# Kernel tuning notes

Hardware: AMD Instinct MI355X
Metric: run time of the kernel (lower is better)

The kernel has to match this reference:

```python
import jax, jax.numpy as jnp
import numpy as np

EMB_DIM = 1024
HEAD_DIM = 64


def setup_inputs() -> dict:
    key = jax.random.key(0)
    kx, kq, kk, kv = jax.random.split(key, 4)
    B, S = 4, 4096
    x = jax.random.normal(kx, (B, S, EMB_DIM), dtype=jnp.float32)
    # nn.Linear weights are [out, in]; kaiming-uniform-ish init scale
    lim = 1.0 / np.sqrt(EMB_DIM)
    Wq = jax.random.uniform(kq, (HEAD_DIM, EMB_DIM), jnp.float32, -lim, lim)
    Wk = jax.random.uniform(kk, (HEAD_DIM, EMB_DIM), jnp.float32, -lim, lim)
    Wv = jax.random.uniform(kv, (HEAD_DIM, EMB_DIM), jnp.float32, -lim, lim)
    return {"x": x, "Wq": Wq, "Wk": Wk, "Wv": Wv}


def reference(x, Wq, Wk, Wv):
    # x: [B, S, E]; W*: [H, E] (torch Linear layout) -> project with x @ W.T
    Q = jnp.einsum("bse,he->bsh", x, Wq)
    K = jnp.einsum("bse,he->bsh", x, Wk)
    V = jnp.einsum("bse,he->bsh", x, Wv)
    # NOTE: source scales by emb_dim**0.5, not head_dim**0.5 — keep faithful.
    scores = jnp.einsum("bqh,bkh->bqk", Q, K) / jnp.sqrt(jnp.float32(x.shape[-1]))
    S = scores.shape[-1]
    causal = jnp.tril(jnp.ones((S, S), dtype=bool))  # [S, S]
    scores = jnp.where(causal, scores, -jnp.inf)
    attn = jax.nn.softmax(scores, axis=-1)
    return jnp.einsum("bqk,bkh->bqh", attn, V)
```

## Files before the change

### kernel.cpp

```cpp
#include <hip/hip_runtime.h>
#include <hip/hip_bf16.h>
#include <math.h>

#define B_ 4
#define S_ 4096
#define E_ 1024

typedef __attribute__((ext_vector_type(8))) short bf16x8;
typedef __attribute__((ext_vector_type(4))) short bf16x4;
typedef __attribute__((ext_vector_type(4))) float f32x4;

__device__ __forceinline__ unsigned short f2bf(float f) {
  unsigned u = __float_as_uint(f);
  u = u + 0x7fffu + ((u >> 16) & 1u);
  return (unsigned short)(u >> 16);
}

__global__ __launch_bounds__(256) void proj_kernel(
    const float* __restrict__ x, const float* __restrict__ Wq,
    const float* __restrict__ Wk, const float* __restrict__ Wv,
    unsigned short* __restrict__ Qp, unsigned short* __restrict__ Kb,
    unsigned short* __restrict__ Vt)
{
  __shared__ __align__(16) unsigned short xs[64*64];
  __shared__ __align__(16) unsigned short wl[192*64];
  const int tid = threadIdx.x;
  const int wave = tid >> 6, lane = tid & 63;
  const int l15 = lane & 15, l4 = lane >> 4;
  const int m0 = blockIdx.x * 64;

  f32x4 acc[12];
  #pragma unroll
  for (int i = 0; i < 12; i++) acc[i] = (f32x4)0.f;

  f32x4 xr[4], wr[12];
  #pragma unroll
  for (int i = 0; i < 4; i++) {
    int c = tid + i*256; int row = c >> 4, cc = c & 15;
    xr[i] = *(const f32x4*)(x + (size_t)(m0 + row)*E_ + cc*4);
  }
  #pragma unroll
  for (int i = 0; i < 12; i++) {
    int c = tid + i*256; int n = c >> 4, cc = c & 15;
    const float* Wsrc = (n < 64) ? (Wq + (size_t)n*E_)
                     : ((n < 128) ? (Wk + (size_t)(n-64)*E_)
                                  : (Wv + (size_t)(n-128)*E_));
    wr[i] = *(const f32x4*)(Wsrc + cc*4);
  }

  for (int ks = 0; ks < 16; ks++) {
    __syncthreads();
    #pragma unroll
    for (int i = 0; i < 4; i++) {
      int c = tid + i*256; int row = c >> 4, cc = c & 15;
      bf16x4 v;
      v[0] = (short)f2bf(xr[i][0]); v[1] = (short)f2bf(xr[i][1]);
      v[2] = (short)f2bf(xr[i][2]); v[3] = (short)f2bf(xr[i][3]);
      *(bf16x4*)((char*)xs + row*128 + ((cc*8) ^ ((row&7)<<4))) = v;
    }
    #pragma unroll
    for (int i = 0; i < 12; i++) {
      int c = tid + i*256; int n = c >> 4, cc = c & 15;
      bf16x4 v;
      v[0] = (short)f2bf(wr[i][0]); v[1] = (short)f2bf(wr[i][1]);
      v[2] = (short)f2bf(wr[i][2]); v[3] = (short)f2bf(wr[i][3]);
      *(bf16x4*)((char*)wl + n*128 + ((cc*8) ^ ((n&7)<<4))) = v;
    }
    if (ks < 15) {
      #pragma unroll
      for (int i = 0; i < 4; i++) {
        int c = tid + i*256; int row = c >> 4, cc = c & 15;
        xr[i] = *(const f32x4*)(x + (size_t)(m0 + row)*E_ + (ks+1)*64 + cc*4);
      }
      #pragma unroll
      for (int i = 0; i < 12; i++) {
        int c = tid + i*256; int n = c >> 4, cc = c & 15;
        const float* Wsrc = (n < 64) ? (Wq + (size_t)n*E_)
                         : ((n < 128) ? (Wk + (size_t)(n-64)*E_)
                                      : (Wv + (size_t)(n-128)*E_));
        wr[i] = *(const f32x4*)(Wsrc + (ks+1)*64 + cc*4);
      }
    }
    __syncthreads();
    const int arow = wave*16 + l15;
    const int aswz = (arow&7)<<4;
    bf16x8 a0 = *(const bf16x8*)((const char*)xs + arow*128 + ((l4*16) ^ aswz));
    bf16x8 a1 = *(const bf16x8*)((const char*)xs + arow*128 + ((64 + l4*16) ^ aswz));
    #pragma unroll
    for (int ntl = 0; ntl < 12; ntl++) {
      int brow = ntl*16 + l15;
      int bswz = (brow&7)<<4;
      bf16x8 b0 = *(const bf16x8*)((const char*)wl + brow*128 + ((l4*16) ^ bswz));
      bf16x8 b1 = *(const bf16x8*)((const char*)wl + brow*128 + ((64 + l4*16) ^ bswz));
      acc[ntl] = __builtin_amdgcn_mfma_f32_16x16x32_bf16(a0, b0, acc[ntl], 0, 0, 0);
      acc[ntl] = __builtin_amdgcn_mfma_f32_16x16x32_bf16(a1, b1, acc[ntl], 0, 0, 0);
    }
  }

  const float QSC = 0.04508422f;
  const int mb = m0 + wave*16 + l4*4;
  #pragma unroll
  for (int ntl = 0; ntl < 4; ntl++) {
    int col = ntl*16 + l15;
    #pragma unroll
    for (int r = 0; r < 4; r++)
      Qp[(size_t)(mb + r)*64 + col] = f2bf(acc[ntl][r] * QSC);
  }
  #pragma unroll
  for (int ntl = 0; ntl < 4; ntl++) {
    int col = ntl*16 + l15;
    #pragma unroll
    for (int r = 0; r < 4; r++)
      Kb[(size_t)(mb + r)*64 + col] = f2bf(acc[4+ntl][r]);
  }
  const int b = m0 >> 12;
  const int sb = (m0 & 4095) + wave*16 + l4*4;
  #pragma unroll
  for (int ntl = 0; ntl < 4; ntl++) {
    int d = ntl*16 + l15;
    bf16x4 v;
    #pragma unroll
    for (int r = 0; r < 4; r++) v[r] = (short)f2bf(acc[8+ntl][r]);
    *(bf16x4*)(Vt + (size_t)(b*64 + d)*S_ + sb) = v;
  }
}

__global__ __launch_bounds__(256) void attn_kernel(
    const unsigned short* __restrict__ Qp,
    const unsigned short* __restrict__ Kb,
    const unsigned short* __restrict__ Vt,
    float* __restrict__ out,
    float* __restrict__ Opart, float* __restrict__ spart, int NS)
{
  __shared__ __align__(16) unsigned short Ks[64*64];
  __shared__ __align__(16) unsigned short Vs[64*64];
  __shared__ __align__(16) float mergeO[4][16][68];
  __shared__ float mstats[4][16][2];

  const int tid = threadIdx.x;
  const int wave = tid >> 6, lane = tid & 63;
  const int l15 = lane & 15, l4 = lane >> 4;
  const int g = wave >> 1, h = wave & 1;

  const int bid = blockIdx.x;
  const int lg = (NS == 4) ? 2 : ((NS == 2) ? 1 : 0);
  const int b  = (bid >> 1) & 3;
  const int ks = (bid >> 3) & (NS - 1);
  const int p  = ((bid >> (3 + lg)) << 1) | (bid & 1);

  const unsigned short* Qb  = Qp + (size_t)b*S_*64;
  const unsigned short* Kbb = Kb + (size_t)b*S_*64;
  const unsigned short* Vtb = Vt + (size_t)b*64*S_;
  float* outb = out + (size_t)b*S_*64;

  #pragma unroll 1
  for (int half = 0; half < 2; half++) {
    const int jq = half ? (127 - p) : p;
    const int q0 = jq * 32;
    const int ntile = (jq >> 1) + 1;
    const int tb = ntile / NS, tr = ntile % NS;
    const int kbeg = ks*tb + (ks < tr ? ks : tr);
    const int kend = kbeg + tb + (ks < tr ? 1 : 0);
    const int qrow = q0 + g*16 + l15;

    bf16x8 qf0 = *(const bf16x8*)(Qb + (size_t)qrow*64 + l4*8);
    bf16x8 qf1 = *(const bf16x8*)(Qb + (size_t)qrow*64 + 32 + l4*8);

    float m = -INFINITY, lsum = 0.f;
    f32x4 acc[4];
    #pragma unroll
    for (int i = 0; i < 4; i++) acc[i] = (f32x4)0.f;

    f32x4 kreg[2], vreg[2];
    if (kbeg < kend) {
      #pragma unroll
      for (int i = 0; i < 2; i++) {
        int c = tid + i*256; int row = c >> 3, cc = c & 7;
        kreg[i] = *(const f32x4*)((const char*)Kbb + (size_t)(kbeg*64 + row)*128 + cc*16);
        vreg[i] = *(const f32x4*)((const char*)Vtb + (size_t)row*8192 + (size_t)kbeg*128 + cc*16);
      }
    }

    for (int t = kbeg; t < kend; t++) {
      __syncthreads();
      #pragma unroll
      for (int i = 0; i < 2; i++) {
        int c = tid + i*256; int row = c >> 3, cc = c & 7;
        *(f32x4*)((char*)Ks + row*128 + ((cc*16) ^ ((row&7)<<4))) = kreg[i];
        *(f32x4*)((char*)Vs + row*128 + ((cc*16) ^ ((row&7)<<4))) = vreg[i];
      }
      if (t + 1 < kend) {
        int k0 = (t+1)*64;
        #pragma unroll
        for (int i = 0; i < 2; i++) {
          int c = tid + i*256; int row = c >> 3, cc = c & 7;
          kreg[i] = *(const f32x4*)((const char*)Kbb + (size_t)(k0+row)*128 + cc*16);
          vreg[i] = *(const f32x4*)((const char*)Vtb + (size_t)row*8192 + (size_t)k0*2 + cc*16);
        }
      }
      __syncthreads();

      f32x4 sv[2];
      #pragma unroll
      for (int st = 0; st < 2; st++) {
        int krow = (2*h + st)*16 + l15;
        const char* kbp = (const char*)Ks + krow*128;
        int swz = (krow&7)<<4;
        bf16x8 k0f = *(const bf16x8*)(kbp + ((l4*16) ^ swz));
        bf16x8 k1f = *(const bf16x8*)(kbp + ((64 + l4*16) ^ swz));
        f32x4 z = (f32x4)0.f;
        z = __builtin_amdgcn_mfma_f32_16x16x32_bf16(k0f, qf0, z, 0, 0, 0);
        z = __builtin_amdgcn_mfma_f32_16x16x32_bf16(k1f, qf1, z, 0, 0, 0);
        sv[st] = z;
      }
      if (t == ntile - 1) {
        #pragma unroll
        for (int st = 0; st < 2; st++) {
          #pragma unroll
          for (int r = 0; r < 4; r++) {
            int kg = t*64 + (2*h + st)*16 + l4*4 + r;
            if (kg > qrow) sv[st][r] = -INFINITY;
          }
        }
      }
      float pmax = sv[0][0];
      #pragma unroll
      for (int st = 0; st < 2; st++) {
        #pragma unroll
        for (int r = 0; r < 4; r++) pmax = fmaxf(pmax, sv[st][r]);
      }
      pmax = fmaxf(pmax, __shfl_xor(pmax, 16, 64));
      pmax = fmaxf(pmax, __shfl_xor(pmax, 32, 64));
      float mnew = fmaxf(m, pmax);
      float msafe = (mnew == -INFINITY) ? 0.f : mnew;
      float scale = exp2f(m - msafe);
      float pv[8]; float psum = 0.f;
      #pragma unroll
      for (int i = 0; i < 8; i++) {
        pv[i] = exp2f(sv[i>>2][i&3] - msafe);
        psum += pv[i];
      }
      psum += __shfl_xor(psum, 16, 64);
      psum += __shfl_xor(psum, 32, 64);
      lsum = lsum*scale + psum;
      m = mnew;
      #pragma unroll
      for (int i = 0; i < 4; i++) acc[i] *= scale;
      bf16x8 pf;
      #pragma unroll
      for (int i = 0; i < 8; i++) pf[i] = (short)f2bf(pv[i]);
      #pragma unroll
      for (int dt = 0; dt < 4; dt++) {
        int drow = dt*16 + l15;
        const char* vb = (const char*)Vs + drow*128;
        int swz = (drow&7)<<4;
        bf16x4 v0 = *(const bf16x4*)(vb + ((h*64 + l4*8) ^ swz));
        bf16x4 v1 = *(const bf16x4*)(vb + ((h*64 + 32 + l4*8) ^ swz));
        bf16x8 vf;
        #pragma unroll
        for (int i = 0; i < 4; i++) { vf[i] = v0[i]; vf[i+4] = v1[i]; }
        acc[dt] = __builtin_amdgcn_mfma_f32_16x16x32_bf16(vf, pf, acc[dt], 0, 0, 0);
      }
    }

    __syncthreads();
    #pragma unroll
    for (int dt = 0; dt < 4; dt++)
      *(f32x4*)&mergeO[wave][l15][dt*16 + l4*4] = acc[dt];
    if (lane < 16) { mstats[wave][lane][0] = m; mstats[wave][lane][1] = lsum; }
    __syncthreads();
    {
      int ql = tid >> 3, dc = tid & 7;
      int gg = ql >> 4, q16 = ql & 15;
      float m1 = mstats[gg*2+0][q16][0], s1 = mstats[gg*2+0][q16][1];
      float m2 = mstats[gg*2+1][q16][0], s2 = mstats[gg*2+1][q16][1];
      float m12 = fmaxf(m1, m2);
      float msafe12 = (m12 == -INFINITY) ? 0.f : m12;
      float a1 = exp2f(m1 - msafe12), a2 = exp2f(m2 - msafe12);
      float s12 = s1*a1 + s2*a2;
      if (NS == 1) {
        float inv = 1.f / s12;
        float b1 = a1*inv, b2 = a2*inv;
        #pragma unroll
        for (int i = 0; i < 2; i++) {
          int d = dc*8 + i*4;
          f32x4 o1 = *(const f32x4*)&mergeO[gg*2+0][q16][d];
          f32x4 o2 = *(const f32x4*)&mergeO[gg*2+1][q16][d];
          f32x4 o = o1*b1 + o2*b2;
          *(f32x4*)(outb + (size_t)(q0 + ql)*64 + d) = o;
        }
      } else {
        int slot = ((b*128 + jq)*NS + ks);
        #pragma unroll
        for (int i = 0; i < 2; i++) {
          int d = dc*8 + i*4;
          f32x4 o1 = *(const f32x4*)&mergeO[gg*2+0][q16][d];
          f32x4 o2 = *(const f32x4*)&mergeO[gg*2+1][q16][d];
          f32x4 o = o1*a1 + o2*a2;
          *(f32x4*)(Opart + (size_t)slot*2048 + ql*64 + d) = o;
        }
        if (dc == 0) {
          spart[(size_t)slot*64 + ql*2]     = m12;
          spart[(size_t)slot*64 + ql*2 + 1] = s12;
        }
      }
    }
  }
}

__global__ __launch_bounds__(256) void merge_kernel(
    const float* __restrict__ Opart, const float* __restrict__ spart,
    float* __restrict__ out, int NS)
{
  const int bid = blockIdx.x;
  const int b = bid >> 7, jq = bid & 127;
  const int q0 = jq * 32;
  const int ql = threadIdx.x >> 3, dc = threadIdx.x & 7;
  const int base = (b*128 + jq) * NS;

  float M = -INFINITY;
  for (int i = 0; i < NS; i++)
    M = fmaxf(M, spart[(size_t)(base+i)*64 + ql*2]);
  float wsum = 0.f;
  f32x4 o0 = (f32x4)0.f, o1 = (f32x4)0.f;
  for (int i = 0; i < NS; i++) {
    float mi = spart[(size_t)(base+i)*64 + ql*2];
    float li = spart[(size_t)(base+i)*64 + ql*2 + 1];
    float a = exp2f(mi - M);
    wsum += li * a;
    const float* op = Opart + (size_t)(base+i)*2048 + ql*64 + dc*8;
    o0 += a * (*(const f32x4*)op);
    o1 += a * (*(const f32x4*)(op + 4));
  }
  float inv = 1.f / wsum;
  float* dst = out + (size_t)b*S_*64 + (size_t)(q0 + ql)*64 + dc*8;
  *(f32x4*)dst = o0 * inv;
  *(f32x4*)(dst + 4) = o1 * inv;
}

extern "C" void kernel_launch(void* const* d_in, const int* in_sizes, int n_in,
                              void* d_out, int out_size, void* d_ws, size_t ws_size,
                              hipStream_t stream)
{
  const float* x  = (const float*)d_in[0];
  const float* Wq = (const float*)d_in[1];
  const float* Wk = (const float*)d_in[2];
  const float* Wv = (const float*)d_in[3];
  unsigned short* Qp  = (unsigned short*)d_ws;
  unsigned short* Kbp = Qp  + (size_t)B_*S_*64;
  unsigned short* Vtp = Kbp + (size_t)B_*S_*64;
  float* out = (float*)d_out;

  const size_t qkv = (size_t)B_*S_*64*2*3;
  const size_t per_ns = (size_t)512*2048*4 + (size_t)512*64*4;
  int NS = (ws_size >= qkv + 4*per_ns) ? 4
         : (ws_size >= qkv + 2*per_ns) ? 2 : 1;
  float* Opart = (float*)((char*)d_ws + qkv);
  float* spart = (float*)((char*)d_ws + qkv + (size_t)NS*512*2048*4);

  hipLaunchKernelGGL(proj_kernel, dim3(256), dim3(256), 0, stream,
                     x, Wq, Wk, Wv, Qp, Kbp, Vtp);
  hipLaunchKernelGGL(attn_kernel, dim3(256*NS), dim3(256), 0, stream,
                     Qp, Kbp, Vtp, out, Opart, spart, NS);
  if (NS > 1)
    hipLaunchKernelGGL(merge_kernel, dim3(512), dim3(256), 0, stream,
                       Opart, spart, out, NS);
}
```

Measured before the change: 160.7 us.

## Use 64-row query tiles with one wave per 16 rows, drop intra-block merge

Each attention block now covers 64 query rows, with each of the four waves owning 16 rows across the full 64-key tile. Previously pairs of waves split the key tile and merged through shared memory. This removes the shared-memory merge, its extra barriers and the mergeO/mstats buffers, and doubles the reuse of each K/V tile loaded into LDS. The cost is half as many blocks (128*NS) and twice the per-wave softmax work and registers, which may reduce parallelism on the large GPU. The partial buffers and merge kernel layout are changed to match.

```diff
diff --git a/kernel.cpp b/kernel.cpp
--- a/kernel.cpp
+++ b/kernel.cpp
@@ -134,19 +134,17 @@
 {
   __shared__ __align__(16) unsigned short Ks[64*64];
   __shared__ __align__(16) unsigned short Vs[64*64];
-  __shared__ __align__(16) float mergeO[4][16][68];
-  __shared__ float mstats[4][16][2];
 
   const int tid = threadIdx.x;
   const int wave = tid >> 6, lane = tid & 63;
   const int l15 = lane & 15, l4 = lane >> 4;
-  const int g = wave >> 1, h = wave & 1;
+  const int g = wave;
 
   const int bid = blockIdx.x;
   const int lg = (NS == 4) ? 2 : ((NS == 2) ? 1 : 0);
-  const int b  = (bid >> 1) & 3;
-  const int ks = (bid >> 3) & (NS - 1);
-  const int p  = ((bid >> (3 + lg)) << 1) | (bid & 1);
+  const int b  = bid & 3;
+  const int ks = (bid >> 2) & (NS - 1);
+  const int p  = bid >> (2 + lg);
 
   const unsigned short* Qb  = Qp + (size_t)b*S_*64;
   const unsigned short* Kbb = Kb + (size_t)b*S_*64;
@@ -155,9 +153,9 @@
 
   #pragma unroll 1
   for (int half = 0; half < 2; half++) {
-    const int jq = half ? (127 - p) : p;
-    const int q0 = jq * 32;
-    const int ntile = (jq >> 1) + 1;
+    const int jq = half ? (63 - p) : p;
+    const int q0 = jq * 64;
+    const int ntile = jq + 1;
     const int tb = ntile / NS, tr = ntile % NS;
     const int kbeg = ks*tb + (ks < tr ? ks : tr);
     const int kend = kbeg + tb + (ks < tr ? 1 : 0);
@@ -190,20 +188,19 @@
         *(f32x4*)((char*)Vs + row*128 + ((cc*16) ^ ((row&7)<<4))) = vreg[i];
       }
       if (t + 1 < kend) {
-        int k0 = (t+1)*64;
         #pragma unroll
         for (int i = 0; i < 2; i++) {
           int c = tid + i*256; int row = c >> 3, cc = c & 7;
-          kreg[i] = *(const f32x4*)((const char*)Kbb + (size_t)(k0+row)*128 + cc*16);
-          vreg[i] = *(const f32x4*)((const char*)Vtb + (size_t)row*8192 + (size_t)k0*2 + cc*16);
+          kreg[i] = *(const f32x4*)((const char*)Kbb + (size_t)((t+1)*64 + row)*128 + cc*16);
+          vreg[i] = *(const f32x4*)((const char*)Vtb + (size_t)row*8192 + (size_t)(t+1)*128 + cc*16);
         }
       }
       __syncthreads();
 
-      f32x4 sv[2];
-      #pragma unroll
-      for (int st = 0; st < 2; st++) {
-        int krow = (2*h + st)*16 + l15;
+      f32x4 sv[4];
+      #pragma unroll
+      for (int kt = 0; kt < 4; kt++) {
+        int krow = kt*16 + l15;
         const char* kbp = (const char*)Ks + krow*128;
         int swz = (krow&7)<<4;
         bf16x8 k0f = *(const bf16x8*)(kbp + ((l4*16) ^ swz));
@@ -211,32 +208,32 @@
         f32x4 z = (f32x4)0.f;
         z = __builtin_amdgcn_mfma_f32_16x16x32_bf16(k0f, qf0, z, 0, 0, 0);
         z = __builtin_amdgcn_mfma_f32_16x16x32_bf16(k1f, qf1, z, 0, 0, 0);
-        sv[st] = z;
+        sv[kt] = z;
       }
       if (t == ntile - 1) {
         #pragma unroll
-        for (int st = 0; st < 2; st++) {
+        for (int kt = 0; kt < 4; kt++) {
           #pragma unroll
           for (int r = 0; r < 4; r++) {
-            int kg = t*64 + (2*h + st)*16 + l4*4 + r;
-            if (kg > qrow) sv[st][r] = -INFINITY;
+            int kg = t*64 + kt*16 + l4*4 + r;
+            if (kg > qrow) sv[kt][r] = -INFINITY;
           }
         }
       }
       float pmax = sv[0][0];
       #pragma unroll
-      for (int st = 0; st < 2; st++) {
+      for (int kt = 0; kt < 4; kt++) {
         #pragma unroll
-        for (int r = 0; r < 4; r++) pmax = fmaxf(pmax, sv[st][r]);
+        for (int r = 0; r < 4; r++) pmax = fmaxf(pmax, sv[kt][r]);
       }
       pmax = fmaxf(pmax, __shfl_xor(pmax, 16, 64));
       pmax = fmaxf(pmax, __shfl_xor(pmax, 32, 64));
       float mnew = fmaxf(m, pmax);
       float msafe = (mnew == -INFINITY) ? 0.f : mnew;
       float scale = exp2f(m - msafe);
-      float pv[8]; float psum = 0.f;
-      #pragma unroll
-      for (int i = 0; i < 8; i++) {
+      float pv[16]; float psum = 0.f;
+      #pragma unroll
+      for (int i = 0; i < 16; i++) {
         pv[i] = exp2f(sv[i>>2][i&3] - msafe);
         psum += pv[i];
       }
@@ -246,63 +243,43 @@
       m = mnew;
       #pragma unroll
       for (int i = 0; i < 4; i++) acc[i] *= scale;
-      bf16x8 pf;
-      #pragma unroll
-      for (int i = 0; i < 8; i++) pf[i] = (short)f2bf(pv[i]);
+      bf16x8 pf0, pf1;
+      #pragma unroll
+      for (int i = 0; i < 8; i++) { pf0[i] = (short)f2bf(pv[i]); pf1[i] = (short)f2bf(pv[8+i]); }
       #pragma unroll
       for (int dt = 0; dt < 4; dt++) {
         int drow = dt*16 + l15;
         const char* vb = (const char*)Vs + drow*128;
         int swz = (drow&7)<<4;
-        bf16x4 v0 = *(const bf16x4*)(vb + ((h*64 + l4*8) ^ swz));
-        bf16x4 v1 = *(const bf16x4*)(vb + ((h*64 + 32 + l4*8) ^ swz));
-        bf16x8 vf;
+        bf16x4 a0 = *(const bf16x4*)(vb + ((l4*8) ^ swz));
+        bf16x4 a1 = *(const bf16x4*)(vb + ((32 + l4*8) ^ swz));
+        bf16x4 a2 = *(const bf16x4*)(vb + ((64 + l4*8) ^ swz));
+        bf16x4 a3 = *(const bf16x4*)(vb + ((96 + l4*8) ^ swz));
+        bf16x8 vf0, vf1;
         #pragma unroll
-        for (int i = 0; i < 4; i++) { vf[i] = v0[i]; vf[i+4] = v1[i]; }
-        acc[dt] = __builtin_amdgcn_mfma_f32_16x16x32_bf16(vf, pf, acc[dt], 0, 0, 0);
-      }
-    }
-
-    __syncthreads();
-    #pragma unroll
-    for (int dt = 0; dt < 4; dt++)
-      *(f32x4*)&mergeO[wave][l15][dt*16 + l4*4] = acc[dt];
-    if (lane < 16) { mstats[wave][lane][0] = m; mstats[wave][lane][1] = lsum; }
-    __syncthreads();
-    {
-      int ql = tid >> 3, dc = tid & 7;
-      int gg = ql >> 4, q16 = ql & 15;
-      float m1 = mstats[gg*2+0][q16][0], s1 = mstats[gg*2+0][q16][1];
-      float m2 = mstats[gg*2+1][q16][0], s2 = mstats[gg*2+1][q16][1];
-      float m12 = fmaxf(m1, m2);
-      float msafe12 = (m12 == -INFINITY) ? 0.f : m12;
-      float a1 = exp2f(m1 - msafe12), a2 = exp2f(m2 - msafe12);
-      float s12 = s1*a1 + s2*a2;
-      if (NS == 1) {
-        float inv = 1.f / s12;
-        float b1 = a1*inv, b2 = a2*inv;
-        #pragma unroll
-        for (int i = 0; i < 2; i++) {
-          int d = dc*8 + i*4;
-          f32x4 o1 = *(const f32x4*)&mergeO[gg*2+0][q16][d];
-          f32x4 o2 = *(const f32x4*)&mergeO[gg*2+1][q16][d];
-          f32x4 o = o1*b1 + o2*b2;
-          *(f32x4*)(outb + (size_t)(q0 + ql)*64 + d) = o;
+        for (int i = 0; i < 4; i++) {
+          vf0[i] = a0[i]; vf0[i+4] = a1[i];
+          vf1[i] = a2[i]; vf1[i+4] = a3[i];
         }
-      } else {
-        int slot = ((b*128 + jq)*NS + ks);
-        #pragma unroll
-        for (int i = 0; i < 2; i++) {
-          int d = dc*8 + i*4;
-          f32x4 o1 = *(const f32x4*)&mergeO[gg*2+0][q16][d];
-          f32x4 o2 = *(const f32x4*)&mergeO[gg*2+1][q16][d];
-          f32x4 o = o1*a1 + o2*a2;
-          *(f32x4*)(Opart + (size_t)slot*2048 + ql*64 + d) = o;
-        }
-        if (dc == 0) {
-          spart[(size_t)slot*64 + ql*2]     = m12;
-          spart[(size_t)slot*64 + ql*2 + 1] = s12;
-        }
+        acc[dt] = __builtin_amdgcn_mfma_f32_16x16x32_bf16(vf0, pf0, acc[dt], 0, 0, 0);
+        acc[dt] = __builtin_amdgcn_mfma_f32_16x16x32_bf16(vf1, pf1, acc[dt], 0, 0, 0);
+      }
+    }
+
+    if (NS == 1) {
+      float inv = 1.f / lsum;
+      #pragma unroll
+      for (int dt = 0; dt < 4; dt++)
+        *(f32x4*)(outb + (size_t)qrow*64 + dt*16 + l4*4) = acc[dt] * inv;
+    } else {
+      int slot = (b*64 + jq)*NS + ks;
+      float* Ob = Opart + (size_t)slot*4096 + (g*16 + l15)*64;
+      #pragma unroll
+      for (int dt = 0; dt < 4; dt++)
+        *(f32x4*)(Ob + dt*16 + l4*4) = acc[dt];
+      if (l4 == 0) {
+        spart[(size_t)slot*128 + (g*16 + l15)*2]     = m;
+        spart[(size_t)slot*128 + (g*16 + l15)*2 + 1] = lsum;
       }
     }
   }
@@ -313,29 +290,33 @@
     float* __restrict__ out, int NS)
 {
   const int bid = blockIdx.x;
-  const int b = bid >> 7, jq = bid & 127;
-  const int q0 = jq * 32;
-  const int ql = threadIdx.x >> 3, dc = threadIdx.x & 7;
-  const int base = (b*128 + jq) * NS;
+  const int b = bid & 3, jq = bid >> 2;
+  const int q = threadIdx.x >> 2;
+  const int dq = threadIdx.x & 3;
+  const int base = (b*64 + jq) * NS;
 
   float M = -INFINITY;
   for (int i = 0; i < NS; i++)
-    M = fmaxf(M, spart[(size_t)(base+i)*64 + ql*2]);
+    M = fmaxf(M, spart[(size_t)(base+i)*128 + q*2]);
   float wsum = 0.f;
-  f32x4 o0 = (f32x4)0.f, o1 = (f32x4)0.f;
+  f32x4 o0 = (f32x4)0.f, o1 = (f32x4)0.f, o2 = (f32x4)0.f, o3 = (f32x4)0.f;
   for (int i = 0; i < NS; i++) {
-    float mi = spart[(size_t)(base+i)*64 + ql*2];
-    float li = spart[(size_t)(base+i)*64 + ql*2 + 1];
+    float mi = spart[(size_t)(base+i)*128 + q*2];
+    float li = spart[(size_t)(base+i)*128 + q*2 + 1];
     float a = exp2f(mi - M);
     wsum += li * a;
-    const float* op = Opart + (size_t)(base+i)*2048 + ql*64 + dc*8;
+    const float* op = Opart + (size_t)(base+i)*4096 + q*64 + dq*16;
     o0 += a * (*(const f32x4*)op);
     o1 += a * (*(const f32x4*)(op + 4));
+    o2 += a * (*(const f32x4*)(op + 8));
+    o3 += a * (*(const f32x4*)(op + 12));
   }
   float inv = 1.f / wsum;
-  float* dst = out + (size_t)b*S_*64 + (size_t)(q0 + ql)*64 + dc*8;
-  *(f32x4*)dst = o0 * inv;
+  float* dst = out + (size_t)b*S_*64 + (size_t)(jq*64 + q)*64 + dq*16;
+  *(f32x4*)dst       = o0 * inv;
   *(f32x4*)(dst + 4) = o1 * inv;
+  *(f32x4*)(dst + 8) = o2 * inv;
+  *(f32x4*)(dst + 12)= o3 * inv;
 }
 
 extern "C" void kernel_launch(void* const* d_in, const int* in_sizes, int n_in,
@@ -352,17 +333,17 @@
   float* out = (float*)d_out;
 
   const size_t qkv = (size_t)B_*S_*64*2*3;
-  const size_t per_ns = (size_t)512*2048*4 + (size_t)512*64*4;
+  const size_t per_ns = (size_t)256*4096*4 + (size_t)256*128*4;
   int NS = (ws_size >= qkv + 4*per_ns) ? 4
          : (ws_size >= qkv + 2*per_ns) ? 2 : 1;
   float* Opart = (float*)((char*)d_ws + qkv);
-  float* spart = (float*)((char*)d_ws + qkv + (size_t)NS*512*2048*4);
+  float* spart = (float*)((char*)d_ws + qkv + (size_t)NS*256*4096*4);
 
   hipLaunchKernelGGL(proj_kernel, dim3(256), dim3(256), 0, stream,
                      x, Wq, Wk, Wv, Qp, Kbp, Vtp);
-  hipLaunchKernelGGL(attn_kernel, dim3(256*NS), dim3(256), 0, stream,
+  hipLaunchKernelGGL(attn_kernel, dim3(4*32*NS), dim3(256), 0, stream,
                      Qp, Kbp, Vtp, out, Opart, spart, NS);
   if (NS > 1)
-    hipLaunchKernelGGL(merge_kernel, dim3(512), dim3(256), 0, stream,
+    hipLaunchKernelGGL(merge_kernel, dim3(256), dim3(256), 0, stream,
                        Opart, spart, out, NS);
 }
```

After: 154.5 us. -3.9%, faster.
